# Optimization experiments

Measured on AMD Instinct MI355X. Metric: run time of the kernel, lower is better.

## Reference

```python
import jax, jax.numpy as jnp
import numpy as np

N_INP = 256
N_OUT = 16
H = 1024
UH = 32  # uni_hidden_unit
BATCH = 16384


def setup_inputs() -> dict:
    key = jax.random.key(0)
    ks = jax.random.split(key, 16)
    s = 0.02
    return {
        "x": jax.random.normal(ks[0], (BATCH, N_INP), dtype=jnp.float32),
        # main MLP: n_inp -> 1024 -> 1024 -> n_out
        "W0": jax.random.normal(ks[1], (N_INP, H), dtype=jnp.float32) * s,
        "b0": jnp.zeros((H,), jnp.float32),
        "W1": jax.random.normal(ks[2], (H, H), dtype=jnp.float32) * s,
        "b1": jnp.zeros((H,), jnp.float32),
        "W2": jax.random.normal(ks[3], (H, N_OUT), dtype=jnp.float32) * s,
        "b2": jnp.zeros((N_OUT,), jnp.float32),
        # stacked per-feature uni MLPs: 1 -> UH -> UH -> n_out, one per feature
        "uw1": jax.random.normal(ks[4], (N_INP, UH), dtype=jnp.float32) * s,
        "ub1": jnp.zeros((N_INP, UH), jnp.float32),
        "uw2": jax.random.normal(ks[5], (N_INP, UH, UH), dtype=jnp.float32) * s,
        "ub2": jnp.zeros((N_INP, UH), jnp.float32),
        "uw3": jax.random.normal(ks[6], (N_INP, UH, N_OUT), dtype=jnp.float32) * s,
        "ub3": jnp.zeros((N_INP, N_OUT), jnp.float32),
    }


def reference(x, W0, b0, W1, b1, W2, b2, uw1, ub1, uw2, ub2, uw3, ub3):
    # main MLP: Linear+ReLU, Linear+ReLU, Linear
    y = jax.nn.relu(x @ W0 + b0)
    y = jax.nn.relu(y @ W1 + b1)
    y = y @ W2 + b2  # [B, n_out]

    # per-feature univariate MLPs, vectorized over the feature axis i
    # input to uni MLP i is x[:, i:i+1]  -> first Linear(1, UH)
    h = jax.nn.relu(x[:, :, None] * uw1[None] + ub1[None])       # [B, I, UH]
    h = jax.nn.relu(jnp.einsum('bif,ifo->bio', h, uw2) + ub2[None])  # [B, I, UH]
    u = jnp.einsum('bif,ifo->bio', h, uw3) + ub3[None]           # [B, I, n_out]
    return y + u.sum(axis=1)
```

## Files before the change

### kernel.cpp

```cpp
#include <hip/hip_runtime.h>

typedef unsigned short u16;
typedef __attribute__((ext_vector_type(4))) float f32x4;
typedef __attribute__((ext_vector_type(4))) int i32x4;
typedef __attribute__((ext_vector_type(8))) __bf16 bf16x8;
typedef __attribute__((ext_vector_type(4))) unsigned short u16x4;

#define BATCH 16384
#define NINP 256
#define HID 1024
#define NOUT 16

__device__ __forceinline__ u16 f2bf(float f) {
  unsigned u = __builtin_bit_cast(unsigned, f);
  u += 0x7FFFu + ((u >> 16) & 1u);
  return (u16)(u >> 16);
}
__device__ __forceinline__ f32x4 mfma_bb(bf16x8 a, bf16x8 b, f32x4 c) {
  return __builtin_amdgcn_mfma_f32_16x16x32_bf16(a, b, c, 0, 0, 0);
}
__device__ __forceinline__ void gload_lds16(const void* g, void* l) {
  __builtin_amdgcn_global_load_lds(
      (const __attribute__((address_space(1))) void*)g,
      (__attribute__((address_space(3))) void*)l, 16, 0, 0);
}

static const size_t OFF_H0    = 0;
static const size_t OFF_PARTU = 0;
static const size_t OFF_XB    = 33554432;
static const size_t OFF_PARTF = 33554432;
static const size_t OFF_W0T   = 67108864;
static const size_t OFF_W1T   = 67633152;
static const size_t OFF_W2T   = 69730304;
static const size_t OFF_UWP   = 69763072;
static const size_t OFF_CB    = 70811648;

__global__ __launch_bounds__(256) void k_prep(
    const float* __restrict__ x,
    const float* __restrict__ W0, const float* __restrict__ W1,
    const float* __restrict__ W2,
    const float* __restrict__ uw1, const float* __restrict__ ub1,
    const float* __restrict__ uw2, const float* __restrict__ ub2,
    const float* __restrict__ uw3, const float* __restrict__ b2,
    const float* __restrict__ ub3,
    u16* __restrict__ xb,
    u16* __restrict__ W0T, u16* __restrict__ W1T, u16* __restrict__ W2T,
    char* __restrict__ uwp, float* __restrict__ cb)
{
  __shared__ float tile[32][33];
  const int bid = blockIdx.x;
  const int tid = threadIdx.x;

  if (bid < 1312) {
    const float* src; u16* dst; int K, N, kb, ob;
    if (bid < 256)       { src = W0; dst = W0T; K = 256;  N = 1024; int t = bid;        kb = (t & 7) * 32;  ob = (t >> 3) * 32; }
    else if (bid < 1280) { src = W1; dst = W1T; K = 1024; N = 1024; int t = bid - 256;  kb = (t & 31) * 32; ob = (t >> 5) * 32; }
    else                 { src = W2; dst = W2T; K = 1024; N = 16;   int t = bid - 1280; kb = t * 32;        ob = 0; }
    const int tx = tid & 31, ty = tid >> 5;
    for (int r = ty; r < 32; r += 8)
      if (ob + tx < N) tile[r][tx] = src[(size_t)(kb + r) * N + ob + tx];
    __syncthreads();
    for (int r = ty; r < 32; r += 8)
      if (ob + r < N) dst[(size_t)(ob + r) * K + kb + tx] = f2bf(tile[tx][r]);
  } else if (bid < 5408) {
    const int idx = ((bid - 1312) * 256 + tid) * 4;
    const float4 v = *(const float4*)&x[idx];
    u16x4 o4 = { f2bf(v.x), f2bf(v.y), f2bf(v.z), f2bf(v.w) };
    *(u16x4*)&xb[idx] = o4;
  } else if (bid < 5664) {
    const int e = ((bid - 5408) * 256 + tid) * 4;
    const float4 v = *(const float4*)&uw2[e];
    const int i = e >> 10, f = (e >> 5) & 31, o = e & 31;
    const float vv[4] = { v.x, v.y, v.z, v.w };
    u16* blob16 = (u16*)(uwp + (size_t)i * 4096);
#pragma unroll
    for (int d = 0; d < 4; ++d) {
      const int oo = o + d;
      const int lane = ((f >> 3) << 4) | (oo & 15);
      blob16[256 + (oo >> 4) * 512 + lane * 8 + (f & 7)] = f2bf(vv[d]);
    }
  } else if (bid < 5792) {
    const int e = ((bid - 5664) * 256 + tid) * 4;
    const float4 v = *(const float4*)&uw3[e];
    const int i = e >> 9, f = (e >> 4) & 31, o2 = e & 15;
    const int s = (f < 16) ? (((f >> 2) << 3) + (f & 3))
                           : ((((f - 16) >> 2) << 3) + 4 + (f & 3));
    const float vv[4] = { v.x, v.y, v.z, v.w };
    u16* blob16 = (u16*)(uwp + (size_t)i * 4096);
#pragma unroll
    for (int d = 0; d < 4; ++d)
      blob16[1280 + ((s >> 3) * 16 + o2 + d) * 8 + (s & 7)] = f2bf(vv[d]);
  } else if (bid < 5816) {
    const int e4 = (bid - 5792) * 256 + tid;
    const int i = e4 / 24, r4 = e4 % 24;
    const float* src = (r4 < 8)  ? &uw1[i * 32 + r4 * 4]
                     : (r4 < 16) ? &ub1[i * 32 + (r4 - 8) * 4]
                                 : &ub2[i * 32 + (r4 - 16) * 4];
    *(float4*)(uwp + (size_t)i * 4096 + r4 * 16) = *(const float4*)src;
  } else {
    __shared__ float red[16][16];
    const int ig = tid >> 4, o = tid & 15;
    float s = 0.f;
#pragma unroll
    for (int k = 0; k < 16; ++k) s += ub3[(ig * 16 + k) * 16 + o];
    red[ig][o] = s;
    __syncthreads();
    if (tid < 16) {
      float t = b2[tid];
#pragma unroll
      for (int k = 0; k < 16; ++k) t += red[k][tid];
      cb[tid] = t;
    }
  }
}

template<int KT, bool FOLD>
__device__ __forceinline__ void gemm_body(
    const u16* __restrict__ A, const u16* __restrict__ BT,
    const float* __restrict__ bias, u16* __restrict__ C,
    const u16* __restrict__ W2Tp, float* __restrict__ pfold, int N)
{
  extern __shared__ __align__(16) char lds[];
  const int tid = threadIdx.x;
  const int lane = tid & 63, wid = tid >> 6;
  const int l15 = lane & 15, g = lane >> 4;
  const int wA = wid >> 2;
  const int wn = wid & 3;
  const int nbn = N >> 8;
  int logical = blockIdx.x;
  { const int nwg = gridDim.x;
    if ((nwg & 7) == 0) { const int q = nwg >> 3; logical = (logical & 7) * q + (logical >> 3); } }
  const int bm = logical / nbn, bn = logical - bm * nbn;
  const size_t rb = (size_t)bm * 256, cb = (size_t)bn * 256;

  const int q7 = l15 & 7;
  const int arow0 = wA * 128 + l15;
  const int brow0 = wn * 64 + l15;

  char* const ldsA = lds;
  char* const ldsB = lds + 65536;

  const u16* Ag = A + rb * KT;
  const u16* Bg = BT + cb * KT;

  bf16x8 w2f[8];
  if constexpr (FOLD) {
#pragma unroll
    for (int c = 0; c < 8; ++c)
      w2f[c] = __builtin_bit_cast(bf16x8,
          *(const i32x4*)&W2Tp[l15 * HID + (int)cb + c * 32 + g * 8]);
  }
  float bv[4];
#pragma unroll
  for (int n = 0; n < 4; ++n) bv[n] = bias[cb + wn * 64 + n * 16 + l15];

  f32x4 acc[8][4] = {};
  const int NT = KT >> 6;

#define STAGE(arr, src, ktE, s) do { \
    const int G_ = (s) * 512 + tid; \
    const int row_ = G_ >> 3; \
    const int c8_ = (G_ & 7) ^ (row_ & 7); \
    gload_lds16(&(src)[(size_t)row_ * KT + (ktE) + c8_ * 8], (arr) + G_ * 16); \
  } while (0)

#define ARD(bp, m, kk) (*(const bf16x8*)((bp) + (((arow0 + (m) * 16) * 8 + (((kk) * 4 + g) ^ q7)) << 4)))
#define BRD(bp, n, kk) (*(const bf16x8*)((bp) + (((brow0 + (n) * 16) * 8 + (((kk) * 4 + g) ^ q7)) << 4)))

#define KTILE(Ab, Bb, An, Bn, kt1, LASTT) do {                                 \
    bf16x8 av[4][2], bv0[2][2], bv1[2][2];                                     \
                 \
    _Pragma("unroll")                                                          \
    for (int m = 0; m < 4; ++m) { av[m][0] = ARD(Ab, m, 0); av[m][1] = ARD(Ab, m, 1); } \
    _Pragma("unroll")                                                          \
    for (int n = 0; n < 2; ++n) { bv0[n][0] = BRD(Bb, n, 0); bv0[n][1] = BRD(Bb, n, 1); } \
    if (!(LASTT)) { STAGE(Bn, Bg, kt1, 0); STAGE(Bn, Bg, kt1, 1);              \
                    STAGE(Bn, Bg, kt1, 2); STAGE(Bn, Bg, kt1, 3); }            \
    asm volatile("s_waitcnt lgkmcnt(8)" ::: "memory");                         \
    __builtin_amdgcn_s_barrier();                                              \
    asm volatile("s_waitcnt lgkmcnt(0)" ::: "memory");                         \
    __builtin_amdgcn_s_setprio(1);                                             \
    _Pragma("unroll")                                                          \
    for (int m = 0; m < 4; ++m)                                                \
      _Pragma("unroll")                                                        \
      for (int n = 0; n < 2; ++n) {                                            \
        acc[m][n] = mfma_bb(av[m][0], bv0[n][0], acc[m][n]);                   \
        acc[m][n] = mfma_bb(av[m][1], bv0[n][1], acc[m][n]);                   \
      }                                                                        \
    __builtin_amdgcn_s_setprio(0);                                             \
    __builtin_amdgcn_s_barrier();                                              \
    \
    _Pragma("unroll")                                                          \
    for (int n = 0; n < 2; ++n) { bv1[n][0] = BRD(Bb, n + 2, 0); bv1[n][1] = BRD(Bb, n + 2, 1); } \
    if (!(LASTT)) { STAGE(An, Ag, kt1, 0); STAGE(An, Ag, kt1, 2);              \
                    STAGE(An, Ag, kt1, 1); STAGE(An, Ag, kt1, 3); }            \
    __builtin_amdgcn_s_barrier();                                              \
    asm volatile("s_waitcnt lgkmcnt(0)" ::: "memory");                         \
    __builtin_amdgcn_s_setprio(1);                                             \
    _Pragma("unroll")                                                          \
    for (int m = 0; m < 4; ++m)                                                \
      _Pragma("unroll")                                                        \
      for (int n = 0; n < 2; ++n) {                                            \
        acc[m][n + 2] = mfma_bb(av[m][0], bv1[n][0], acc[m][n + 2]);           \
        acc[m][n + 2] = mfma_bb(av[m][1], bv1[n][1], acc[m][n + 2]);           \
      }                                                                        \
    __builtin_amdgcn_s_setprio(0);                                             \
    if (LASTT) { asm volatile("s_waitcnt vmcnt(0)" ::: "memory"); }            \
    else       { asm volatile("s_waitcnt vmcnt(8)" ::: "memory"); }            \
    __builtin_amdgcn_s_barrier();                                              \
                                          \
    _Pragma("unroll")                                                          \
    for (int m = 0; m < 4; ++m) { av[m][0] = ARD(Ab, m + 4, 0); av[m][1] = ARD(Ab, m + 4, 1); } \
    __builtin_amdgcn_s_barrier();                                              \
    asm volatile("s_waitcnt lgkmcnt(0)" ::: "memory");                         \
    __builtin_amdgcn_s_setprio(1);                                             \
    _Pragma("unroll")                                                          \
    for (int m = 0; m < 4; ++m)                                                \
      _Pragma("unroll")                                                        \
      for (int n = 0; n < 2; ++n) {                                            \
        acc[m + 4][n + 2] = mfma_bb(av[m][0], bv1[n][0], acc[m + 4][n + 2]);   \
        acc[m + 4][n + 2] = mfma_bb(av[m][1], bv1[n][1], acc[m + 4][n + 2]);   \
      }                                                                        \
    __builtin_amdgcn_s_setprio(0);                                             \
    __builtin_amdgcn_s_barrier();                                              \
        \
    __builtin_amdgcn_s_setprio(1);                                             \
    _Pragma("unroll")                                                          \
    for (int m = 0; m < 4; ++m)                                                \
      _Pragma("unroll")                                                        \
      for (int n = 0; n < 2; ++n) {                                            \
        acc[m + 4][n] = mfma_bb(av[m][0], bv0[n][0], acc[m + 4][n]);           \
        acc[m + 4][n] = mfma_bb(av[m][1], bv0[n][1], acc[m + 4][n]);           \
      }                                                                        \
    __builtin_amdgcn_s_setprio(0);                                             \
    if (!(LASTT)) { asm volatile("s_waitcnt vmcnt(2)" ::: "memory"); }         \
    __builtin_amdgcn_s_barrier();                                              \
  } while (0)

  STAGE(ldsB, Bg, 0, 0); STAGE(ldsB, Bg, 0, 1);
  STAGE(ldsB, Bg, 0, 2); STAGE(ldsB, Bg, 0, 3);
  STAGE(ldsA, Ag, 0, 0); STAGE(ldsA, Ag, 0, 2);
  STAGE(ldsA, Ag, 0, 1); STAGE(ldsA, Ag, 0, 3);
  asm volatile("s_waitcnt vmcnt(2)" ::: "memory");
  __builtin_amdgcn_s_barrier();

  for (int t = 0; t < NT - 1; ++t) {
    const int b = t & 1;
    KTILE(ldsA + b * 32768, ldsB + b * 32768,
          ldsA + (b ^ 1) * 32768, ldsB + (b ^ 1) * 32768,
          (t + 1) << 6, false);
  }
  {
    const int b = (NT - 1) & 1;
    KTILE(ldsA + b * 32768, ldsB + b * 32768,
          ldsA + (b ^ 1) * 32768, ldsB + (b ^ 1) * 32768, 0, true);
  }
#undef KTILE
#undef STAGE
#undef ARD
#undef BRD

  asm volatile("s_waitcnt vmcnt(0)" ::: "memory");

  {
    char* const ep = lds;
#pragma unroll
    for (int h = 0; h < 2; ++h) {
      __syncthreads();
#pragma unroll
      for (int mloc = 0; mloc < 4; ++mloc)
#pragma unroll
        for (int n = 0; n < 4; ++n) {
          const int col = wn * 64 + n * 16 + l15;
#pragma unroll
          for (int r = 0; r < 4; ++r) {
            const int lrow = wA * 64 + mloc * 16 + g * 4 + r;
            *(u16*)(ep + lrow * 512 + ((col * 2) ^ ((lrow & 7) << 4))) =
                f2bf(fmaxf(acc[h * 4 + mloc][n][r] + bv[n], 0.f));
          }
        }
      __syncthreads();
      if constexpr (!FOLD) {
#pragma unroll
        for (int p = 0; p < 8; ++p) {
          const int ci = p * 512 + tid;
          const int lrow = ci >> 5, c16 = ci & 31;
          const i32x4 v = *(const i32x4*)(ep + lrow * 512 + ((c16 * 16) ^ ((lrow & 7) << 4)));
          const int grow = (int)rb + (lrow >> 6) * 128 + h * 64 + (lrow & 63);
          *(i32x4*)&C[(size_t)grow * N + cb + c16 * 8] = v;
        }
      } else {
        const int lrow = wid * 16 + l15;
        f32x4 accf = {0.f, 0.f, 0.f, 0.f};
#pragma unroll
        for (int c = 0; c < 8; ++c) {
          const bf16x8 afr = *(const bf16x8*)(
              ep + lrow * 512 + ((c * 64 + g * 16) ^ ((lrow & 7) << 4)));
          accf = mfma_bb(afr, w2f[c], accf);
        }
        const int rowb2 = (int)rb + (wid >> 2) * 128 + h * 64 + (wid & 3) * 16;
        float* pf = pfold + ((size_t)bn * BATCH + rowb2) * NOUT;
#pragma unroll
        for (int r = 0; r < 4; ++r)
          pf[(g * 4 + r) * NOUT + l15] = accf[r];
      }
    }
  }
}

__global__ __launch_bounds__(512, 2) void k_g1(
    const u16* __restrict__ A, const u16* __restrict__ BT,
    const float* __restrict__ bias, u16* __restrict__ C, int N)
{
  gemm_body<256, false>(A, BT, bias, C, nullptr, nullptr, N);
}
__global__ __launch_bounds__(512, 2) void k_g2(
    const u16* __restrict__ A, const u16* __restrict__ BT,
    const float* __restrict__ bias, const u16* __restrict__ W2Tp,
    float* __restrict__ pfold, int N)
{
  gemm_body<1024, true>(A, BT, bias, nullptr, W2Tp, pfold, N);
}

__global__ __launch_bounds__(256, 4) void k_uni(
    const float* __restrict__ x,
    const char* __restrict__ uwp,
    float* __restrict__ part)
{
  const int tid = threadIdx.x, lane = tid & 63, wid = tid >> 6;
  const int l15 = lane & 15, g = lane >> 4;
  const int chunk = blockIdx.x & 7, rowblk = blockIdx.x >> 3;
  const int rb_blk = rowblk * 128;
  const int rb = rb_blk + wid * 32;
  const int i0 = chunk * 32;

  __shared__ __align__(16) float xt[128][33];
  __shared__ __align__(16) char wbuf[3][4096];

  {
    const int r0 = tid >> 3, c4 = (tid & 7) << 2;
#pragma unroll
    for (int rr = 0; rr < 128; rr += 32)
      *(float4*)&xt[rr + r0][c4] =
          *(const float4*)&x[(size_t)(rb_blk + rr + r0) * NINP + i0 + c4];
  }
  gload_lds16(uwp + (size_t)i0 * 4096 + tid * 16, &wbuf[0][tid * 16]);
  gload_lds16(uwp + (size_t)(i0 + 1) * 4096 + tid * 16, &wbuf[1][tid * 16]);
  __syncthreads();

  const f32x4 zero4 = {0.f, 0.f, 0.f, 0.f};
  f32x4 acc0 = zero4, acc1 = zero4;
  const float* xr0 = &xt[wid * 32 + l15][0];
  const float* xr1 = &xt[wid * 32 + 16 + l15][0];

#pragma unroll 2
  for (int ii = 0; ii < 32; ++ii) {
    const int nf = i0 + ((ii + 2) & 31);
    gload_lds16(uwp + (size_t)nf * 4096 + tid * 16,
                &wbuf[(ii + 2) % 3][tid * 16]);

    const char* bp = &wbuf[ii % 3][0];
    const f32x4 w1lo = *(const f32x4*)(bp + g * 32);
    const f32x4 w1hi = *(const f32x4*)(bp + g * 32 + 16);
    const f32x4 b1lo = *(const f32x4*)(bp + 128 + g * 32);
    const f32x4 b1hi = *(const f32x4*)(bp + 128 + g * 32 + 16);
    const f32x4 bb0  = *(const f32x4*)(bp + 256 + g * 16);
    const f32x4 bb1  = *(const f32x4*)(bp + 320 + g * 16);
    const bf16x8 bv0 = *(const bf16x8*)(bp + 512 + lane * 16);
    const bf16x8 bv1 = *(const bf16x8*)(bp + 1536 + lane * 16);
    const bf16x8 b3  = *(const bf16x8*)(bp + 2560 + lane * 16);
    const float xv0 = xr0[ii], xv1 = xr1[ii];

    bf16x8 af0, af1;
#pragma unroll
    for (int j = 0; j < 4; ++j) {
      af0[j]     = (__bf16)fmaxf(fmaf(xv0, w1lo[j], b1lo[j]), 0.f);
      af0[4 + j] = (__bf16)fmaxf(fmaf(xv0, w1hi[j], b1hi[j]), 0.f);
      af1[j]     = (__bf16)fmaxf(fmaf(xv1, w1lo[j], b1lo[j]), 0.f);
      af1[4 + j] = (__bf16)fmaxf(fmaf(xv1, w1hi[j], b1hi[j]), 0.f);
    }

    const f32x4 d00 = mfma_bb(bv0, af0, bb0);
    const f32x4 d10 = mfma_bb(bv1, af0, bb1);
    const f32x4 d01 = mfma_bb(bv0, af1, bb0);
    const f32x4 d11 = mfma_bb(bv1, af1, bb1);

    bf16x8 h20, h21;
#pragma unroll
    for (int j = 0; j < 4; ++j) {
      h20[j]     = (__bf16)fmaxf(d00[j], 0.f);
      h20[4 + j] = (__bf16)fmaxf(d10[j], 0.f);
      h21[j]     = (__bf16)fmaxf(d01[j], 0.f);
      h21[4 + j] = (__bf16)fmaxf(d11[j], 0.f);
    }

    acc0 = mfma_bb(b3, h20, acc0);
    acc1 = mfma_bb(b3, h21, acc1);

    asm volatile("s_waitcnt vmcnt(1)" ::: "memory");
    __builtin_amdgcn_s_barrier();
  }

  float* p = part + ((size_t)chunk * BATCH + rb) * NOUT;
  *(f32x4*)&p[l15 * 16 + g * 4] = acc0;
  *(f32x4*)&p[(16 + l15) * 16 + g * 4] = acc1;
}

__global__ __launch_bounds__(256) void k_reduce(
    const float* __restrict__ pu, const float* __restrict__ pf,
    const float* __restrict__ cb, float* __restrict__ out)
{
  const int j4 = blockIdx.x * 256 + threadIdx.x;
  const float4 c = ((const float4*)cb)[j4 & 3];
  const float4* a4 = (const float4*)pu;
  const float4* b4 = (const float4*)pf;
  float rx = c.x, ry = c.y, rz = c.z, rw = c.w;
#pragma unroll
  for (int cc = 0; cc < 8; ++cc) {
    const float4 a = a4[cc * 65536 + j4];
    rx += a.x; ry += a.y; rz += a.z; rw += a.w;
  }
#pragma unroll
  for (int cc = 0; cc < 4; ++cc) {
    const float4 a = b4[cc * 65536 + j4];
    rx += a.x; ry += a.y; rz += a.z; rw += a.w;
  }
  float4 r; r.x = rx; r.y = ry; r.z = rz; r.w = rw;
  ((float4*)out)[j4] = r;
}

extern "C" void kernel_launch(void* const* d_in, const int* in_sizes, int n_in,
                              void* d_out, int out_size, void* d_ws, size_t ws_size,
                              hipStream_t stream) {
  (void)in_sizes; (void)n_in; (void)out_size; (void)ws_size;
  const float* x   = (const float*)d_in[0];
  const float* W0  = (const float*)d_in[1];
  const float* b0  = (const float*)d_in[2];
  const float* W1  = (const float*)d_in[3];
  const float* b1  = (const float*)d_in[4];
  const float* W2  = (const float*)d_in[5];
  const float* b2  = (const float*)d_in[6];
  const float* uw1 = (const float*)d_in[7];
  const float* ub1 = (const float*)d_in[8];
  const float* uw2 = (const float*)d_in[9];
  const float* ub2 = (const float*)d_in[10];
  const float* uw3 = (const float*)d_in[11];
  const float* ub3 = (const float*)d_in[12];
  float* out = (float*)d_out;

  char* ws = (char*)d_ws;
  u16*   H0    = (u16*)(ws + OFF_H0);
  u16*   xb    = (u16*)(ws + OFF_XB);
  u16*   W0T   = (u16*)(ws + OFF_W0T);
  u16*   W1T   = (u16*)(ws + OFF_W1T);
  u16*   W2T   = (u16*)(ws + OFF_W2T);
  char*  uwp   = (char*)(ws + OFF_UWP);
  float* cb    = (float*)(ws + OFF_CB);
  float* partu = (float*)(ws + OFF_PARTU);
  float* partf = (float*)(ws + OFF_PARTF);

  hipFuncSetAttribute((const void*)k_g1,
                      hipFuncAttributeMaxDynamicSharedMemorySize, 131072);
  hipFuncSetAttribute((const void*)k_g2,
                      hipFuncAttributeMaxDynamicSharedMemorySize, 131072);

  k_prep<<<5817, 256, 0, stream>>>(x, W0, W1, W2, uw1, ub1, uw2, ub2, uw3,
                                   b2, ub3, xb, W0T, W1T, W2T, uwp, cb);
  k_g1<<<256, 512, 131072, stream>>>(xb, W0T, b0, H0, HID);
  k_g2<<<256, 512, 131072, stream>>>(H0, W1T, b1, W2T, partf, HID);
  k_uni<<<1024, 256, 0, stream>>>(x, uwp, partu);
  k_reduce<<<256, 256, 0, stream>>>(partu, partf, cb, out);
}
```

Baseline: 98.10 us.

## Collapse four-phase GEMM k-tile schedule into two phases with fewer barriers

Restructures the bf16 MFMA k-tile loop body. All eight global-to-LDS prefetch stages for the next tile are now issued at the start. The B fragments for all four n-subtiles are read up front, and the MFMAs run in two larger phases (rows 0-3, then rows 4-7). This drops four of the six per-tile barriers, the explicit lgkmcnt waits and the s_setprio priority toggling, aiming to cut synchronisation overhead. In exchange it loses the interleaved ping-pong scheduling between waves and keeps more fragment registers live at once.

```diff
diff --git a/kernel.cpp b/kernel.cpp
--- a/kernel.cpp
+++ b/kernel.cpp
@@ -169,72 +169,42 @@
 
 #define KTILE(Ab, Bb, An, Bn, kt1, LASTT) do {                                 \
     bf16x8 av[4][2], bv0[2][2], bv1[2][2];                                     \
-                 \
+              \
+    if (!(LASTT)) { STAGE(Bn, Bg, kt1, 0); STAGE(Bn, Bg, kt1, 1);              \
+                    STAGE(Bn, Bg, kt1, 2); STAGE(Bn, Bg, kt1, 3);              \
+                    STAGE(An, Ag, kt1, 0); STAGE(An, Ag, kt1, 2);              \
+                    STAGE(An, Ag, kt1, 1); STAGE(An, Ag, kt1, 3); }            \
     _Pragma("unroll")                                                          \
     for (int m = 0; m < 4; ++m) { av[m][0] = ARD(Ab, m, 0); av[m][1] = ARD(Ab, m, 1); } \
     _Pragma("unroll")                                                          \
-    for (int n = 0; n < 2; ++n) { bv0[n][0] = BRD(Bb, n, 0); bv0[n][1] = BRD(Bb, n, 1); } \
-    if (!(LASTT)) { STAGE(Bn, Bg, kt1, 0); STAGE(Bn, Bg, kt1, 1);              \
-                    STAGE(Bn, Bg, kt1, 2); STAGE(Bn, Bg, kt1, 3); }            \
-    asm volatile("s_waitcnt lgkmcnt(8)" ::: "memory");                         \
-    __builtin_amdgcn_s_barrier();                                              \
-    asm volatile("s_waitcnt lgkmcnt(0)" ::: "memory");                         \
-    __builtin_amdgcn_s_setprio(1);                                             \
+    for (int n = 0; n < 2; ++n) { bv0[n][0] = BRD(Bb, n, 0); bv0[n][1] = BRD(Bb, n, 1); \
+                                  bv1[n][0] = BRD(Bb, n + 2, 0); bv1[n][1] = BRD(Bb, n + 2, 1); } \
     _Pragma("unroll")                                                          \
     for (int m = 0; m < 4; ++m)                                                \
       _Pragma("unroll")                                                        \
       for (int n = 0; n < 2; ++n) {                                            \
-        acc[m][n] = mfma_bb(av[m][0], bv0[n][0], acc[m][n]);                   \
-        acc[m][n] = mfma_bb(av[m][1], bv0[n][1], acc[m][n]);                   \
+        acc[m][n]     = mfma_bb(av[m][0], bv0[n][0], acc[m][n]);               \
+        acc[m][n]     = mfma_bb(av[m][1], bv0[n][1], acc[m][n]);               \
+        acc[m][n + 2] = mfma_bb(av[m][0], bv1[n][0], acc[m][n + 2]);           \
+        acc[m][n + 2] = mfma_bb(av[m][1], bv1[n][1], acc[m][n + 2]);           \
       }                                                                        \
-    __builtin_amdgcn_s_setprio(0);                                             \
-    __builtin_amdgcn_s_barrier();                                              \
-    \
+    if (LASTT) { asm volatile("s_waitcnt vmcnt(0)" ::: "memory"); }            \
+    else       { asm volatile("s_waitcnt vmcnt(8)" ::: "memory"); }            \
+    asm volatile("s_barrier" ::: "memory");                                    \
+                                             \
     _Pragma("unroll")                                                          \
-    for (int n = 0; n < 2; ++n) { bv1[n][0] = BRD(Bb, n + 2, 0); bv1[n][1] = BRD(Bb, n + 2, 1); } \
-    if (!(LASTT)) { STAGE(An, Ag, kt1, 0); STAGE(An, Ag, kt1, 2);              \
-                    STAGE(An, Ag, kt1, 1); STAGE(An, Ag, kt1, 3); }            \
-    __builtin_amdgcn_s_barrier();                                              \
-    asm volatile("s_waitcnt lgkmcnt(0)" ::: "memory");                         \
-    __builtin_amdgcn_s_setprio(1);                                             \
+    for (int m = 0; m < 4; ++m) { av[m][0] = ARD(Ab, m + 4, 0); av[m][1] = ARD(Ab, m + 4, 1); } \
     _Pragma("unroll")                                                          \
     for (int m = 0; m < 4; ++m)                                                \
       _Pragma("unroll")                                                        \
       for (int n = 0; n < 2; ++n) {                                            \
-        acc[m][n + 2] = mfma_bb(av[m][0], bv1[n][0], acc[m][n + 2]);           \
-        acc[m][n + 2] = mfma_bb(av[m][1], bv1[n][1], acc[m][n + 2]);           \
-      }                                                                        \
-    __builtin_amdgcn_s_setprio(0);                                             \
-    if (LASTT) { asm volatile("s_waitcnt vmcnt(0)" ::: "memory"); }            \
-    else       { asm volatile("s_waitcnt vmcnt(8)" ::: "memory"); }            \
-    __builtin_amdgcn_s_barrier();                                              \
-                                          \
-    _Pragma("unroll")                                                          \
-    for (int m = 0; m < 4; ++m) { av[m][0] = ARD(Ab, m + 4, 0); av[m][1] = ARD(Ab, m + 4, 1); } \
-    __builtin_amdgcn_s_barrier();                                              \
-    asm volatile("s_waitcnt lgkmcnt(0)" ::: "memory");                         \
-    __builtin_amdgcn_s_setprio(1);                                             \
-    _Pragma("unroll")                                                          \
-    for (int m = 0; m < 4; ++m)                                                \
-      _Pragma("unroll")                                                        \
-      for (int n = 0; n < 2; ++n) {                                            \
+        acc[m + 4][n]     = mfma_bb(av[m][0], bv0[n][0], acc[m + 4][n]);       \
+        acc[m + 4][n]     = mfma_bb(av[m][1], bv0[n][1], acc[m + 4][n]);       \
         acc[m + 4][n + 2] = mfma_bb(av[m][0], bv1[n][0], acc[m + 4][n + 2]);   \
         acc[m + 4][n + 2] = mfma_bb(av[m][1], bv1[n][1], acc[m + 4][n + 2]);   \
       }                                                                        \
-    __builtin_amdgcn_s_setprio(0);                                             \
-    __builtin_amdgcn_s_barrier();                                              \
-        \
-    __builtin_amdgcn_s_setprio(1);                                             \
-    _Pragma("unroll")                                                          \
-    for (int m = 0; m < 4; ++m)                                                \
-      _Pragma("unroll")                                                        \
-      for (int n = 0; n < 2; ++n) {                                            \
-        acc[m + 4][n] = mfma_bb(av[m][0], bv0[n][0], acc[m + 4][n]);           \
-        acc[m + 4][n] = mfma_bb(av[m][1], bv0[n][1], acc[m + 4][n]);           \
-      }                                                                        \
-    __builtin_amdgcn_s_setprio(0);                                             \
     if (!(LASTT)) { asm volatile("s_waitcnt vmcnt(2)" ::: "memory"); }         \
-    __builtin_amdgcn_s_barrier();                                              \
+    asm volatile("s_barrier" ::: "memory");                                    \
   } while (0)
 
   STAGE(ldsB, Bg, 0, 0); STAGE(ldsB, Bg, 0, 1);
@@ -242,7 +212,7 @@
   STAGE(ldsA, Ag, 0, 0); STAGE(ldsA, Ag, 0, 2);
   STAGE(ldsA, Ag, 0, 1); STAGE(ldsA, Ag, 0, 3);
   asm volatile("s_waitcnt vmcnt(2)" ::: "memory");
-  __builtin_amdgcn_s_barrier();
+  asm volatile("s_barrier" ::: "memory");
 
   for (int t = 0; t < NT - 1; ++t) {
     const int b = t & 1;
```

After: 97.71 us. No clear change (-0.4%).
